# Kernel optimization log

Measured on AMD Instinct MI355X. Metric: run time of the kernel, lower is better.

Reference implementation:

```python
import jax, jax.numpy as jnp
import numpy as np
from jax import lax

EPS = 1e-7  # keras backend epsilon used by K.ctc_batch_cost
NEG = -1e30  # log-space 'zero'


def setup_inputs() -> dict:
    key = jax.random.key(0)
    k1, k2 = jax.random.split(key)
    B, T, C, L = 512, 512, 128, 48
    # softmax-like probabilities over classes (ctc_batch_cost expects probs)
    u = jax.random.uniform(k1, (B, T, C), dtype=jnp.float32, minval=1e-3, maxval=1.0)
    y_pred = u / jnp.sum(u, axis=-1, keepdims=True)
    # labels in [0, C-2]; blank index is C-1 (keras convention)
    y_true = jax.random.randint(k2, (B, L), 0, C - 1, dtype=jnp.int64)
    return {"y_true": y_true, "y_pred": y_pred}


def _ctc_loss(y_true, y_pred):
    # y_true: [B, L] int labels; y_pred: [B, T, C] probabilities
    B, T, C = y_pred.shape
    L = y_true.shape[1]
    S = 2 * L + 1
    blank = C - 1

    log_probs = jnp.log(y_pred + EPS)  # [B, T, C]

    # extended label sequence: blank, l1, blank, l2, ..., blank -> [B, S]
    ext = jnp.full((B, S), blank, dtype=y_true.dtype).at[:, 1::2].set(y_true)
    ext_m2 = jnp.concatenate(
        [jnp.full((B, 2), -1, dtype=ext.dtype), ext[:, :-2]], axis=1
    )
    # skip-transition allowed iff current symbol is a non-blank differing from s-2
    skip = (ext != blank) & (ext != ext_m2)  # [B, S]

    # gather per-extended-symbol log probs: [B, T, S] -> time-major [T, B, S]
    lp_ext = jnp.take_along_axis(log_probs, ext[:, None, :], axis=2)
    lp_ext = jnp.moveaxis(lp_ext, 1, 0)

    neg = jnp.asarray(NEG, log_probs.dtype)
    alpha0 = jnp.full((B, S), neg)
    alpha0 = alpha0.at[:, 0].set(lp_ext[0, :, 0]).at[:, 1].set(lp_ext[0, :, 1])

    def step(alpha, lp_t):
        a1 = alpha
        a2 = jnp.concatenate([jnp.full((B, 1), neg), alpha[:, :-1]], axis=1)
        a3 = jnp.concatenate([jnp.full((B, 2), neg), alpha[:, :-2]], axis=1)
        a3 = jnp.where(skip, a3, neg)
        new = jnp.logaddexp(jnp.logaddexp(a1, a2), a3) + lp_t
        return new, None

    alpha_T, _ = lax.scan(step, alpha0, lp_ext[1:])
    # total log-likelihood ends in last blank or last label
    loglik = jnp.logaddexp(alpha_T[:, -1], alpha_T[:, -2])
    return -loglik[:, None]  # [B, 1] like K.ctc_batch_cost


def reference(y_true, y_pred):
    return _ctc_loss(y_true, y_pred)
```

## Files before the change

### kernel.cpp

```cpp
#include <hip/hip_runtime.h>


constexpr int Bc = 512, Tc = 512, Cc = 128, Lc = 48;
constexpr float FEPS = 1e-7f;
constexpr float FNEG = -1e30f;
constexpr float LN2F = 0.69314718055994530942f;
constexpr int CDEAD = -(1 << 28);
constexpr int NG = 16;
constexpr int RD = 8;

#define DPP_WAVE_SHR1 0x138
#define DPP_WAVE_SHL1 0x130
#define WG __HIP_MEMORY_SCOPE_WORKGROUP

__device__ __forceinline__ float dppf_shr1(float x) {
    return __int_as_float(__builtin_amdgcn_update_dpp(
        0, __float_as_int(x), DPP_WAVE_SHR1, 0xF, 0xF, false));
}
__device__ __forceinline__ float dppf_shl1(float x) {
    return __int_as_float(__builtin_amdgcn_update_dpp(
        0, __float_as_int(x), DPP_WAVE_SHL1, 0xF, 0xF, false));
}
__device__ __forceinline__ int dppi_shr1_self(int c) {
    return __builtin_amdgcn_update_dpp(c, c, DPP_WAVE_SHR1, 0xF, 0xF, false);
}
__device__ __forceinline__ int dppi_shl1_self(int c) {
    return __builtin_amdgcn_update_dpp(c, c, DPP_WAVE_SHL1, 0xF, 0xF, false);
}
__device__ __forceinline__ float lae2(float a, float b) {
    float m = fmaxf(a, b);
    float d = fabsf(a - b);
    return m + __log2f(1.0f + __builtin_amdgcn_exp2f(-d));
}
__device__ __forceinline__ float rd63f(float v) {
    return __uint_as_float((unsigned)
        __builtin_amdgcn_readlane(__float_as_uint(v), 63));
}

typedef const __attribute__((address_space(1))) void* gptr_t;
typedef __attribute__((address_space(3))) void* lptr_t;
__device__ __forceinline__ void gload(const float* g, float* l) {
    __builtin_amdgcn_global_load_lds((gptr_t)g, (lptr_t)l, 4, 0, 0);
}

__global__ __launch_bounds__(256)
void ctc_pc_kernel(const int* __restrict__ y_true,
                   const float* __restrict__ y_pred,
                   float* __restrict__ out) {
    const int b = blockIdx.x;
    const int tid = threadIdx.x;
    const int lane = tid & 63;
    const int wid = tid >> 6;

    __shared__ float ring[2][RD][16][64];
    __shared__ int ready[2], done[2];
    __shared__ float sblo[64], sbhi[64];
    __shared__ int sbc[64];

    const float* yb = y_pred + (size_t)b * Tc * Cc;
    const int lab = (lane < Lc) ? y_true[b * Lc + lane] : (Cc - 1);

    if (tid == 0) { ready[0] = ready[1] = 0; done[0] = done[1] = 0; }
    __syncthreads();

    if (wid >= 2) {
        const int d = wid - 2;
        #pragma unroll 1
        for (int g = 0; g < NG; ++g) {
            if (g >= RD) {
                while (__hip_atomic_load(&done[d], __ATOMIC_RELAXED, WG) < g - (RD - 1))
                    __builtin_amdgcn_s_sleep(1);
            }
            float* lb = &ring[d][g & (RD - 1)][0][0];
            const int t0 = d ? (511 - g * 16) : (g * 16);
            #pragma unroll
            for (int j = 0; j < 16; ++j) {
                const int t = d ? (t0 - j) : (t0 + j);
                gload(yb + (size_t)t * Cc + lab, lb + j * 64);
            }
            if (g >= 3) {
                asm volatile("s_waitcnt vmcnt(48)" ::: "memory");
                __builtin_amdgcn_sched_barrier(0);
                if (lane == 0)
                    __hip_atomic_store(&ready[d], g - 2, __ATOMIC_RELAXED, WG);
                __builtin_amdgcn_sched_barrier(0);
            }
        }
        asm volatile("s_waitcnt vmcnt(32)" ::: "memory");
        __builtin_amdgcn_sched_barrier(0);
        if (lane == 0) __hip_atomic_store(&ready[d], NG - 2, __ATOMIC_RELAXED, WG);
        asm volatile("s_waitcnt vmcnt(16)" ::: "memory");
        __builtin_amdgcn_sched_barrier(0);
        if (lane == 0) __hip_atomic_store(&ready[d], NG - 1, __ATOMIC_RELAXED, WG);
        asm volatile("s_waitcnt vmcnt(0)" ::: "memory");
        __builtin_amdgcn_sched_barrier(0);
        if (lane == 0) __hip_atomic_store(&ready[d], NG, __ATOMIC_RELAXED, WG);
    } else {
        const int dir = wid;
        const int labm1 = __builtin_amdgcn_ds_bpermute(((lane + 63) & 63) << 2, lab);
        const bool skip = (lab != (Cc - 1)) && (lab != labm1);
        const bool validhi = (lane < Lc);
        const bool lane0 = (lane == 0);

        float lo = 0.0f, hi = 0.0f;
        int c = CDEAD;

        auto renorm = [&]() {
            float mx = fmaxf(lo, hi);
            int e = (int)((__float_as_uint(mx) >> 23) & 0xFF) - 127;
            e = (mx > 0.0f) ? e : 0;
            lo = ldexpf(lo, -e);
            hi = ldexpf(hi, -e);
            c += e;
        };

        float praw[16], pbf[16], phf[16];

        if (dir == 1) {
            lo = (lane == 48) ? 1.0f : 0.0f;
            hi = (lane == 47) ? 1.0f : 0.0f;
            c  = (lane == 47 || lane == 48) ? 0 : CDEAD;
        }

        #pragma unroll 1
        for (int g = 0; g < NG; ++g) {
            while (__hip_atomic_load(&ready[dir], __ATOMIC_RELAXED, WG) < g + 1)
                __builtin_amdgcn_s_sleep(1);
            __builtin_amdgcn_sched_barrier(0);
            #pragma unroll
            for (int j = 0; j < 16; ++j) praw[j] = ring[dir][g & (RD - 1)][j][lane];
            #pragma unroll
            for (int j = 0; j < 16; ++j) {
                pbf[j] = rd63f(praw[j]) + FEPS;
                phf[j] = validhi ? (praw[j] + FEPS) : 0.0f;
            }
            if (dir == 0) {
                int j0 = 0;
                if (g == 0) {
                    lo = lane0 ? pbf[0] : 0.0f;
                    hi = lane0 ? phf[0] : 0.0f;
                    c  = lane0 ? 0 : CDEAD;
                    j0 = 1;
                }
                #pragma unroll
                for (int j = 0; j < 16; ++j) {
                    if (j < j0) continue;
                    float sh  = dppf_shr1(hi);
                    int   cm1 = dppi_shr1_self(c);
                    bool  own_dead = (lo == 0.0f) && (hi == 0.0f);
                    int   m  = own_dead ? cm1 : ((c > cm1) ? c : cm1);
                    float lov = ldexpf(lo, c - m);
                    float hiv = ldexpf(hi, c - m);
                    float shv = ldexpf(sh, cm1 - m);
                    float a3  = skip ? shv : 0.0f;
                    lo = (lov + shv) * pbf[j];
                    hi = (hiv + lov + a3) * phf[j];
                    c = m;
                    if (j == 7 || j == 15) renorm();
                }
            } else {
                #pragma unroll
                for (int j = 0; j < 16; ++j) {
                    float qlo = lo * pbf[j];
                    float qhi = hi * phf[j];
                    float u   = qlo + (skip ? qhi : 0.0f);
                    float un  = dppf_shl1(u);
                    int   cp1 = dppi_shl1_self(c);
                    bool  own_dead = (qlo == 0.0f) && (qhi == 0.0f);
                    int   m  = own_dead ? cp1 : ((c > cp1) ? c : cp1);
                    lo = ldexpf(qlo + qhi, c - m);
                    hi = ldexpf(qhi, c - m) + ldexpf(un, cp1 - m);
                    c = m;
                    if (j == 7 || j == 15) renorm();
                }
            }
            __builtin_amdgcn_sched_barrier(0);
            if (lane == 0)
                __hip_atomic_store(&done[dir], g + 1, __ATOMIC_RELAXED, WG);
        }

        if (dir == 1) {
            sblo[lane] = lo;
            sbhi[lane] = hi;
            sbc[lane]  = c;
        } else {
        }
        __syncthreads();
        if (dir == 0) {
            float blo = sblo[lane], bhi = sbhi[lane];
            float ctot = (float)(c + sbc[lane]);
            float plo = lo * blo;
            float phi = hi * bhi;
            float yl = (plo > 0.0f) ? (__log2f(plo) + ctot) : FNEG;
            float yh = (phi > 0.0f) ? (__log2f(phi) + ctot) : FNEG;
            float v = lae2(yl, yh);
            #pragma unroll
            for (int mk = 1; mk < 64; mk <<= 1)
                v = lae2(v, __shfl_xor(v, mk, 64));
            if (lane0) out[b] = -(v * LN2F);
        }
        return;
    }
    __syncthreads();
}

extern "C" void kernel_launch(void* const* d_in, const int* in_sizes, int n_in,
                              void* d_out, int out_size, void* d_ws, size_t ws_size,
                              hipStream_t stream) {
    const int* y_true = (const int*)d_in[0];
    const float* y_pred = (const float*)d_in[1];
    float* out = (float*)d_out;
    hipLaunchKernelGGL(ctc_pc_kernel, dim3(Bc), dim3(256), 0, stream,
                       y_true, y_pred, out);
}
```

Measured before the change: 32.94 us.

## Load full class rows via 16-byte LDS DMA and gather labels from LDS

The producer waves now copy whole 128-class rows into LDS using 16-byte global_load_lds transfers with coalesced columns, replacing 4-byte per-lane gathers at label offsets. The consumer waves gather label probabilities from the LDS row by label index. The ring depth drops to 4, and the producer keeps three groups in flight, republishing readiness with adjusted vmcnt thresholds. This reduces per-load instruction count and scattered global accesses, at the cost of moving 2x more bytes per time step and risking LDS bank conflicts on the label gather.

```diff
diff --git a/kernel.cpp b/kernel.cpp
--- a/kernel.cpp
+++ b/kernel.cpp
@@ -7,7 +7,7 @@
 constexpr float LN2F = 0.69314718055994530942f;
 constexpr int CDEAD = -(1 << 28);
 constexpr int NG = 16;
-constexpr int RD = 8;
+constexpr int RD = 4;
 
 #define DPP_WAVE_SHR1 0x138
 #define DPP_WAVE_SHL1 0x130
@@ -39,8 +39,8 @@
 
 typedef const __attribute__((address_space(1))) void* gptr_t;
 typedef __attribute__((address_space(3))) void* lptr_t;
-__device__ __forceinline__ void gload(const float* g, float* l) {
-    __builtin_amdgcn_global_load_lds((gptr_t)g, (lptr_t)l, 4, 0, 0);
+__device__ __forceinline__ void gload16(const float* g, float* l) {
+    __builtin_amdgcn_global_load_lds((gptr_t)g, (lptr_t)l, 16, 0, 0);
 }
 
 __global__ __launch_bounds__(256)
@@ -52,7 +52,7 @@
     const int lane = tid & 63;
     const int wid = tid >> 6;
 
-    __shared__ float ring[2][RD][16][64];
+    __shared__ float ring[2][RD][16][Cc];
     __shared__ int ready[2], done[2];
     __shared__ float sblo[64], sbhi[64];
     __shared__ int sbc[64];
@@ -65,36 +65,38 @@
 
     if (wid >= 2) {
         const int d = wid - 2;
+        const int jbase = lane >> 5;
+        const int col = (lane & 31) * 4;
+        auto issue_group = [&](int g) {
+            float* lb = &ring[d][g & (RD - 1)][0][0];
+            #pragma unroll
+            for (int i = 0; i < 8; ++i) {
+                const int step = 2 * i + jbase;
+                const int t = d ? (511 - (g * 16 + step)) : (g * 16 + step);
+                gload16(yb + (size_t)t * Cc + col, lb + i * 2 * Cc);
+            }
+        };
+        auto publish = [&](int v) {
+            __builtin_amdgcn_sched_barrier(0);
+            if (lane == 0)
+                __hip_atomic_store(&ready[d], v, __ATOMIC_RELAXED, WG);
+            __builtin_amdgcn_sched_barrier(0);
+        };
+        issue_group(0); issue_group(1); issue_group(2);
         #pragma unroll 1
-        for (int g = 0; g < NG; ++g) {
-            if (g >= RD) {
-                while (__hip_atomic_load(&done[d], __ATOMIC_RELAXED, WG) < g - (RD - 1))
-                    __builtin_amdgcn_s_sleep(1);
-            }
-            float* lb = &ring[d][g & (RD - 1)][0][0];
-            const int t0 = d ? (511 - g * 16) : (g * 16);
-            #pragma unroll
-            for (int j = 0; j < 16; ++j) {
-                const int t = d ? (t0 - j) : (t0 + j);
-                gload(yb + (size_t)t * Cc + lab, lb + j * 64);
-            }
-            if (g >= 3) {
-                asm volatile("s_waitcnt vmcnt(48)" ::: "memory");
-                __builtin_amdgcn_sched_barrier(0);
-                if (lane == 0)
-                    __hip_atomic_store(&ready[d], g - 2, __ATOMIC_RELAXED, WG);
-                __builtin_amdgcn_sched_barrier(0);
-            }
-        }
-        asm volatile("s_waitcnt vmcnt(32)" ::: "memory");
-        __builtin_amdgcn_sched_barrier(0);
-        if (lane == 0) __hip_atomic_store(&ready[d], NG - 2, __ATOMIC_RELAXED, WG);
+        for (int g = 0; g < NG - 3; ++g) {
+            while (__hip_atomic_load(&done[d], __ATOMIC_RELAXED, WG) < g)
+                __builtin_amdgcn_s_sleep(1);
+            issue_group(g + 3);
+            asm volatile("s_waitcnt vmcnt(24)" ::: "memory");
+            publish(g + 1);
+        }
         asm volatile("s_waitcnt vmcnt(16)" ::: "memory");
-        __builtin_amdgcn_sched_barrier(0);
-        if (lane == 0) __hip_atomic_store(&ready[d], NG - 1, __ATOMIC_RELAXED, WG);
+        publish(NG - 2);
+        asm volatile("s_waitcnt vmcnt(8)" ::: "memory");
+        publish(NG - 1);
         asm volatile("s_waitcnt vmcnt(0)" ::: "memory");
-        __builtin_amdgcn_sched_barrier(0);
-        if (lane == 0) __hip_atomic_store(&ready[d], NG, __ATOMIC_RELAXED, WG);
+        publish(NG);
     } else {
         const int dir = wid;
         const int labm1 = __builtin_amdgcn_ds_bpermute(((lane + 63) & 63) << 2, lab);
@@ -128,7 +130,8 @@
                 __builtin_amdgcn_s_sleep(1);
             __builtin_amdgcn_sched_barrier(0);
             #pragma unroll
-            for (int j = 0; j < 16; ++j) praw[j] = ring[dir][g & (RD - 1)][j][lane];
+            for (int j = 0; j < 16; ++j)
+                praw[j] = ring[dir][g & (RD - 1)][j][lab];
             #pragma unroll
             for (int j = 0; j < 16; ++j) {
                 pbf[j] = rd63f(praw[j]) + FEPS;
@@ -183,7 +186,6 @@
             sblo[lane] = lo;
             sbhi[lane] = hi;
             sbc[lane]  = c;
-        } else {
         }
         __syncthreads();
         if (dir == 0) {
```

New measurement: 36.96 us. 12.2% more time.
